# Kernel tuning notes

Hardware: AMD Instinct MI355X
Metric: run time of the kernel (lower is better)

## Reference

```python
import jax, jax.numpy as jnp
import numpy as np

B, N, D = 64, 577, 768
H = 12
HD = D // H
TOP_K_RATIO = 0.1


def setup_inputs() -> dict:
    key = jax.random.key(0)
    ks = jax.random.split(key, 8)
    s = 1.0 / np.sqrt(D)
    return {
        "x": jax.random.normal(ks[0], (B, N, D), jnp.float32),
        "accumulated_attention": jax.random.uniform(ks[1], (B, N, N), jnp.float32),
        "q_w": jax.random.normal(ks[2], (D, D), jnp.float32) * s,
        "k_w": jax.random.normal(ks[3], (D, D), jnp.float32) * s,
        "v_w": jax.random.normal(ks[4], (D, D), jnp.float32) * s,
        "proj_w": jax.random.normal(ks[5], (D, D), jnp.float32) * s,
        "proj_b": jnp.zeros((D,), jnp.float32),
    }


def reference(x, accumulated_attention, q_w, k_w, v_w, proj_w, proj_b):
    b, n, d = x.shape
    scale = HD ** -0.5
    # CLS-to-patch attention rollout row: (B, N-1)
    cls_attn = accumulated_attention[:, 0, 1:]
    # projections -> (B, H, N, HD)
    q = (x @ q_w.T).reshape(b, n, H, HD).transpose(0, 2, 1, 3)
    k = (x @ k_w.T).reshape(b, n, H, HD).transpose(0, 2, 1, 3)
    v = (x @ v_w.T).reshape(b, n, H, HD).transpose(0, 2, 1, 3)
    # top-k patch selection (+1 for CLS offset), prepend CLS index 0
    kk = max(1, int((n - 1) * TOP_K_RATIO))
    _, top_idx = jax.lax.top_k(cls_attn, kk)
    sel = jnp.concatenate([jnp.zeros((b, 1), top_idx.dtype), top_idx + 1], axis=1)  # (B, K+1)
    # gather selected queries: (B, H, K+1, HD)
    local_q = jnp.take_along_axis(q, sel[:, None, :, None], axis=2)
    # cross-attention of local queries against full K/V
    attn = jax.nn.softmax(jnp.einsum("bhkd,bhnd->bhkn", local_q, k) * scale, axis=-1)
    local_out = jnp.einsum("bhkn,bhnd->bhkd", attn, v)
    local_out = local_out.transpose(0, 2, 1, 3).reshape(b, -1, d)  # (B, K+1, D)
    # scatter back into a copy of x (indices are unique per batch)
    out = x.at[jnp.arange(b)[:, None], sel].set(local_out)
    return out @ proj_w.T + proj_b
```

## Files before the change

### kernel.cpp

```cpp
#include <hip/hip_runtime.h>
#include <stdint.h>

typedef unsigned short u16;
typedef short bf16x8 __attribute__((ext_vector_type(8)));
typedef float f32x4 __attribute__((ext_vector_type(4)));

__device__ __forceinline__ float b2f(u16 u){
  unsigned int i = ((unsigned int)u) << 16;
  return __builtin_bit_cast(float, i);
}
__device__ __forceinline__ u16 f2b(float f){
  unsigned int i = __builtin_bit_cast(unsigned int, f);
  i += 0x7FFFu + ((i >> 16) & 1u);
  return (u16)(i >> 16);
}

__device__ __forceinline__ void async16(const void* g, void* l){
  __builtin_amdgcn_global_load_lds((__attribute__((address_space(1))) void*)(void*)g,
                                   (__attribute__((address_space(3))) void*)l, 16, 0, 0);
}

__global__ void probe_kernel(const u16* __restrict__ qw, int* __restrict__ flag){
  int cnt = 0;
  for (int i = threadIdx.x; i < 4096; i += 64){
    int e = (qw[i] >> 7) & 0xFF;
    cnt += (e >= 140);
  }
#pragma unroll
  for (int off = 32; off; off >>= 1) cnt += __shfl_down(cnt, off);
  if (threadIdx.x == 0) *flag = (cnt > 64) ? 1 : 0;
}

__global__ __launch_bounds__(256) void cvt_kernel(const void* __restrict__ src,
                                                  u16* __restrict__ dst, int n,
                                                  const int* __restrict__ flagp){
  const int i = (blockIdx.x * 256 + threadIdx.x) * 8;
  if (i >= n) return;
  if (*flagp){
    f32x4 a = *(const f32x4*)((const float*)src + i);
    f32x4 b = *(const f32x4*)((const float*)src + i + 4);
    bf16x8 v;
#pragma unroll
    for (int j = 0; j < 4; ++j){ v[j] = (short)f2b(a[j]); v[4+j] = (short)f2b(b[j]); }
    *(bf16x8*)(dst + i) = v;
  } else {
    *(bf16x8*)(dst + i) = *(const bf16x8*)((const u16*)src + i);
  }
}

__global__ __launch_bounds__(256) void cvtw4_kernel(const void* __restrict__ s0,
                                                    const void* __restrict__ s1,
                                                    const void* __restrict__ s2,
                                                    const void* __restrict__ s3,
                                                    u16* __restrict__ dst,
                                                    const int* __restrict__ flagp){
  const int b = blockIdx.x;
  const int wsel = b / 288;
  const int i = (b - wsel*288) * 2048 + threadIdx.x * 8;
  const void* src = (wsel == 0) ? s0 : (wsel == 1) ? s1 : (wsel == 2) ? s2 : s3;
  u16* d = dst + (size_t)wsel * 589824 + i;
  if (*flagp){
    f32x4 a = *(const f32x4*)((const float*)src + i);
    f32x4 c = *(const f32x4*)((const float*)src + i + 4);
    bf16x8 v;
#pragma unroll
    for (int j = 0; j < 4; ++j){ v[j] = (short)f2b(a[j]); v[4+j] = (short)f2b(c[j]); }
    *(bf16x8*)d = v;
  } else {
    *(bf16x8*)d = *(const bf16x8*)((const u16*)src + i);
  }
}

__global__ void cvtb_kernel(const void* __restrict__ src, float* __restrict__ dst,
                            int n, const int* __restrict__ flagp){
  int i = blockIdx.x * 256 + threadIdx.x;
  if (i < n) dst[i] = *flagp ? ((const float*)src)[i] : b2f(((const u16*)src)[i]);
}

__global__ __launch_bounds__(576) void topk_kernel(const void* __restrict__ aa,
                                                   int* __restrict__ qrows,
                                                   const int* __restrict__ flagp){
  const int b = blockIdx.x;
  const int isf32 = *flagp;
  __shared__ float vals[576];
  const int i = threadIdx.x;
  const size_t off = (size_t)b*332929 + 1 + i;
  vals[i] = isf32 ? ((const float*)aa)[off] : b2f(((const u16*)aa)[off]);
  __syncthreads();
  const float vi = vals[i];
  int rank = 0;
  for (int j = 0; j < 576; ++j){
    float vj = vals[j];
    rank += (int)((vj > vi) || (vj == vi && j < i));
  }
  if (rank < 57) qrows[b*58 + 1 + rank] = b*577 + i + 1;
  if (i == 0)    qrows[b*58] = b*577;
}

__global__ __launch_bounds__(256) void gemm_bt(
    const u16* __restrict__ A, const u16* __restrict__ W,
    u16* __restrict__ Ck, u16* __restrict__ Cvt, float* __restrict__ Cout,
    u16* __restrict__ Clq,
    const int* __restrict__ qrows, const float* __restrict__ bias, int mode)
{
  __shared__ __align__(16) u16 As0[4096], As1[4096], As2[4096];
  __shared__ __align__(16) u16 Bs0[4096], Bs1[4096], Bs2[4096];
  const int tid = threadIdx.x;
  const int w = tid >> 6, l = tid & 63;

  int bx, by; bool lqp = false;
  if (mode == 0){
    const int bid = blockIdx.x;
    const int wg = (bid & 7) * 672 + (bid >> 3);
    if (wg < 5202){ bx = wg % 18; by = wg / 18; }
    else { const int t = wg - 5202; bx = t % 6; by = t / 6; lqp = true; }
  } else { bx = blockIdx.x; by = blockIdx.y; }

  const int mBase = by * 128;
  const int nBase = bx * 128;
  const int Meff  = (mode == 0 && !lqp) ? 36928 : 3712;

  const int r0 = tid >> 2;
  const int kc = (((tid & 3) ^ ((r0 >> 1) & 3)) * 8);
  int arow0 = mBase + r0;       if (arow0 > Meff-1) arow0 = Meff-1;
  int arow1 = mBase + 64 + r0;  if (arow1 > Meff-1) arow1 = Meff-1;
  if (mode == 0 && lqp){ arow0 = qrows[arow0]; arow1 = qrows[arow1]; }
  const int wrowBase = (mode == 0 && !lqp) ? (768 + nBase) : nBase;
  const u16* ag0 = A + (size_t)arow0 * 768 + kc;
  const u16* ag1 = A + (size_t)arow1 * 768 + kc;
  const u16* bg0 = W + (size_t)(wrowBase + r0) * 768 + kc;
  const u16* bg1 = W + (size_t)(wrowBase + 64 + r0) * 768 + kc;
  const int toff0 = tid * 8, toff1 = (256 + tid) * 8;

  f32x4 acc[4][4] = {};
  const int wm = (w >> 1) * 64, wn = (w & 1) * 64;
  const int lm = l & 15;
  const int lkx = (((l >> 4) ^ ((l >> 1) & 3)) * 8);

#define STAGE(Ab, Bb, koff) do { \
    async16(ag0 + (koff), &Ab[toff0]); \
    async16(ag1 + (koff), &Ab[toff1]); \
    async16(bg0 + (koff), &Bb[toff0]); \
    async16(bg1 + (koff), &Bb[toff1]); } while(0)

#define COMPUTE(Ab, Bb) { \
    bf16x8 af[4], bfr[4]; \
    _Pragma("unroll") \
    for (int i = 0; i < 4; ++i) af[i]  = *(const bf16x8*)&Ab[(wm + i*16 + lm)*32 + lkx]; \
    _Pragma("unroll") \
    for (int j = 0; j < 4; ++j) bfr[j] = *(const bf16x8*)&Bb[(wn + j*16 + lm)*32 + lkx]; \
    __builtin_amdgcn_s_setprio(1); \
    _Pragma("unroll") \
    for (int i = 0; i < 4; ++i) \
      _Pragma("unroll") \
      for (int j = 0; j < 4; ++j) \
        acc[i][j] = __builtin_amdgcn_mfma_f32_16x16x32_bf16(af[i], bfr[j], acc[i][j], 0, 0, 0); \
    __builtin_amdgcn_s_setprio(0); }

#define VMW4 asm volatile("s_waitcnt vmcnt(4)" ::: "memory")
#define VMW0 asm volatile("s_waitcnt vmcnt(0)" ::: "memory")
#define BAR  __builtin_amdgcn_s_barrier()

  STAGE(As0, Bs0, 0);
  STAGE(As1, Bs1, 32);
#pragma unroll
  for (int u = 0; u < 7; ++u){
    const int kb = u * 96;
    VMW4; BAR; STAGE(As2, Bs2, kb + 64);  COMPUTE(As0, Bs0);
    VMW4; BAR; STAGE(As0, Bs0, kb + 96);  COMPUTE(As1, Bs1);
    VMW4; BAR; STAGE(As1, Bs1, kb + 128); COMPUTE(As2, Bs2);
  }
  VMW4; BAR; STAGE(As2, Bs2, 736); COMPUTE(As0, Bs0);
  VMW4; BAR;                       COMPUTE(As1, Bs1);
  VMW0; BAR;                       COMPUTE(As2, Bs2);

#undef STAGE
#undef COMPUTE
#undef VMW4
#undef VMW0
#undef BAR

  if (mode == 1){
#pragma unroll
    for (int i = 0; i < 4; ++i){
#pragma unroll
      for (int r = 0; r < 4; ++r){
        int m = mBase + wm + i*16 + ((l >> 4) << 2) + r;
        if (m < 3712){
          size_t base = (size_t)qrows[m] * 768;
#pragma unroll
          for (int j = 0; j < 4; ++j){
            int n = nBase + wn + j*16 + lm;
            Cout[base + n] = acc[i][j][r] + bias[n];
          }
        }
      }
    }
    return;
  }
  if (lqp){
#pragma unroll
    for (int i = 0; i < 4; ++i){
#pragma unroll
      for (int r = 0; r < 4; ++r){
        int m = mBase + wm + i*16 + ((l >> 4) << 2) + r;
#pragma unroll
        for (int j = 0; j < 4; ++j){
          int n = nBase + wn + j*16 + lm;
          Clq[(size_t)m*768 + n] = f2b(acc[i][j][r]);
        }
      }
    }
  } else if (nBase < 768){
#pragma unroll
    for (int i = 0; i < 4; ++i){
#pragma unroll
      for (int r = 0; r < 4; ++r){
        int m = mBase + wm + i*16 + ((l >> 4) << 2) + r;
        if (m < 36928){
#pragma unroll
          for (int j = 0; j < 4; ++j){
            int n = nBase + wn + j*16 + lm;
            Ck[(size_t)m*768 + n] = f2b(acc[i][j][r]);
          }
        }
      }
    }
  } else if (nBase < 1536){
#pragma unroll
    for (int i = 0; i < 4; ++i){
#pragma unroll
      for (int r = 0; r < 4; ++r){
        int m = mBase + wm + i*16 + ((l >> 4) << 2) + r;
        if (m < 36928){
          int bb = m / 577;
          int nn = m - bb*577;
#pragma unroll
          for (int j = 0; j < 4; ++j){
            int nf = nBase - 768 + wn + j*16 + lm;
            Cvt[((size_t)(bb*12 + (nf >> 6))*64 + (nf & 63))*608 + nn] = f2b(acc[i][j][r]);
          }
        }
      }
    }
  } else {
#pragma unroll
    for (int i = 0; i < 4; ++i){
#pragma unroll
      for (int r = 0; r < 4; ++r){
        int m = mBase + wm + i*16 + ((l >> 4) << 2) + r;
        if (m < 36928){
          size_t base = (size_t)m * 768;
#pragma unroll
          for (int j = 0; j < 4; ++j){
            int nf = nBase - 1536 + wn + j*16 + lm;
            Cout[base + nf] = acc[i][j][r] + bias[nf];
          }
        }
      }
    }
  }
}

#define SLD 580
__global__ __launch_bounds__(256) void attn_kernel(
    const u16* __restrict__ lq, const u16* __restrict__ K,
    const u16* __restrict__ Vt, u16* __restrict__ lout)
{
  const int bid = blockIdx.x;
  const int wg = (bid & 7) * 384 + (bid >> 3);
  const int mt = wg & 3;
  const int hb = wg >> 2;
  const int h = hb % 12, b = hb / 12;

  __shared__ __align__(16) u16 qs[16*64];
  __shared__ __align__(16) float S[16*SLD];
  float* red = (float*)qs;
  const int tid = threadIdx.x, w = tid >> 6, l = tid & 63;
  const int lm = l & 15, lk = (l >> 4) * 8;

  for (int idx = tid; idx < 1024; idx += 256){
    int r = idx >> 6, c = idx & 63;
    int gm = mt*16 + r;
    qs[idx] = (gm < 58) ? lq[((size_t)b*58 + gm)*768 + h*64 + c] : (u16)0;
  }
  __syncthreads();
  bf16x8 aq0 = *(const bf16x8*)&qs[lm*64 + lk];
  bf16x8 aq1 = *(const bf16x8*)&qs[lm*64 + 32 + lk];

  const u16* Kb = K + (size_t)b*577*768 + h*64;
  for (int t = w; t < 37; t += 4){
    int n0 = t*16;
    int n = n0 + lm; if (n > 576) n = 576;
    const u16* kp = Kb + (size_t)n*768;
    bf16x8 b0 = *(const bf16x8*)&kp[lk];
    bf16x8 b1 = *(const bf16x8*)&kp[32 + lk];
    f32x4 c = {};
    c = __builtin_amdgcn_mfma_f32_16x16x32_bf16(aq0, b0, c, 0, 0, 0);
    c = __builtin_amdgcn_mfma_f32_16x16x32_bf16(aq1, b1, c, 0, 0, 0);
    if (n0 + lm < 577){
#pragma unroll
      for (int r = 0; r < 4; ++r)
        S[(((l >> 4) << 2) + r)*SLD + n0 + lm] = c[r] * 0.125f;
    }
  }
  __syncthreads();

  const int row = tid >> 4, g = tid & 15;
  float mx = -1e30f;
  for (int n = g; n < 577; n += 16) mx = fmaxf(mx, S[row*SLD + n]);
  red[row*17 + g] = mx;
  __syncthreads();
  float m2 = red[row*17];
#pragma unroll
  for (int i = 1; i < 16; ++i) m2 = fmaxf(m2, red[row*17 + i]);
  float sum = 0.f;
  for (int n = g; n < 577; n += 16){
    float e = __expf(S[row*SLD + n] - m2);
    S[row*SLD + n] = e;
    sum += e;
  }
  __syncthreads();
  red[row*17 + g] = sum;
  __syncthreads();
  float s2 = 0.f;
#pragma unroll
  for (int i = 0; i < 16; ++i) s2 += red[row*17 + i];
  float inv = 1.f / s2;
  for (int n = g; n < 577; n += 16) S[row*SLD + n] *= inv;
  __syncthreads();

  const u16* Vb = Vt + ((size_t)(b*12 + h) * 64) * 608;
  f32x4 oc = {};
  for (int ks = 0; ks < 18; ++ks){
    int kb = ks*32 + lk;
    f32x4 p0 = *(const f32x4*)&S[lm*SLD + kb];
    f32x4 p1 = *(const f32x4*)&S[lm*SLD + kb + 4];
    bf16x8 af;
#pragma unroll
    for (int j = 0; j < 4; ++j){ af[j] = (short)f2b(p0[j]); af[4+j] = (short)f2b(p1[j]); }
    bf16x8 bv = *(const bf16x8*)&Vb[(size_t)(w*16 + lm)*608 + kb];
    oc = __builtin_amdgcn_mfma_f32_16x16x32_bf16(af, bv, oc, 0, 0, 0);
  }
  {
    float vt576 = b2f(Vb[(size_t)(w*16 + lm)*608 + 576]);
#pragma unroll
    for (int r = 0; r < 4; ++r)
      oc[r] += S[(((l >> 4) << 2) + r)*SLD + 576] * vt576;
  }
#pragma unroll
  for (int r = 0; r < 4; ++r){
    int ml = mt*16 + ((l >> 4) << 2) + r;
    if (ml < 58)
      lout[((size_t)b*58 + ml)*768 + h*64 + w*16 + lm] = f2b(oc[r]);
  }
}

extern "C" void kernel_launch(void* const* d_in, const int* in_sizes, int n_in,
                              void* d_out, int out_size, void* d_ws, size_t ws_size,
                              hipStream_t stream)
{
  const void* x    = d_in[0];
  const void* aacc = d_in[1];
  const void* q_w  = d_in[2];
  const void* k_w  = d_in[3];
  const void* v_w  = d_in[4];
  const void* p_w  = d_in[5];
  const void* p_b  = d_in[6];

  const int M  = 36928;
  const int Ms = 3712;
  const int XE = M * 768;
  const int WE = 768 * 768;

  u16* Kbuf = (u16*)d_ws;
  u16* Vt   = Kbuf + (size_t)M * 768;
  u16* lq   = Vt + (size_t)768 * 64 * 608;
  u16* lout = lq + (size_t)Ms * 768;
  u16* xb   = lout + (size_t)Ms * 768;
  u16* qwb  = xb + (size_t)XE;
  u16* pwb  = qwb + (size_t)3 * WE;
  float* biasf = (float*)(qwb + (size_t)4 * WE);
  int* qrows = (int*)(biasf + 768);
  int* flagp = qrows + 3712;

  probe_kernel<<<1, 64, 0, stream>>>((const u16*)q_w, flagp);
  cvt_kernel<<<XE/8/256, 256, 0, stream>>>(x, xb, XE, flagp);
  cvtw4_kernel<<<1152, 256, 0, stream>>>(q_w, k_w, v_w, p_w, qwb, flagp);
  cvtb_kernel<<<3, 256, 0, stream>>>(p_b, biasf, 768, flagp);
  topk_kernel<<<64, 576, 0, stream>>>(aacc, qrows, flagp);

  gemm_bt<<<5376, 256, 0, stream>>>(xb, qwb, Kbuf, Vt, (float*)d_out, lq,
                                    qrows, biasf, 0);
  attn_kernel<<<3072, 256, 0, stream>>>(lq, Kbuf, Vt, lout);
  gemm_bt<<<dim3(6, 29), 256, 0, stream>>>(lout, pwb, nullptr, nullptr,
                                           (float*)d_out, nullptr, qrows, biasf, 1);
}
```

Measured before the change: 578.2 us.

## Fuse conversion kernels, widen attention blocks, and retune GEMM scheduling

Merges the probe, x, weight and bias conversion kernels into one prep kernel, with each block re-deriving the fp32/bf16 flag locally. The attention kernel moves to 512 threads: the K-dimension of P·V is split across two wave groups and reduced through shared memory, and softmax normalisation is deferred to the output. The GEMM gets a launch_bounds occupancy hint of 3 and a simpler block-to-tile mapping that separates the local-query tiles. This trades extra redundant flag reads and extra attention syncs for fewer launches and more parallelism.

```diff
diff --git a/kernel.cpp b/kernel.cpp
--- a/kernel.cpp
+++ b/kernel.cpp
@@ -20,68 +20,66 @@
                                    (__attribute__((address_space(3))) void*)l, 16, 0, 0);
 }
 
-__global__ void probe_kernel(const u16* __restrict__ qw, int* __restrict__ flag){
-  int cnt = 0;
-  for (int i = threadIdx.x; i < 4096; i += 64){
-    int e = (qw[i] >> 7) & 0xFF;
-    cnt += (e >= 140);
-  }
-#pragma unroll
-  for (int off = 32; off; off >>= 1) cnt += __shfl_down(cnt, off);
-  if (threadIdx.x == 0) *flag = (cnt > 64) ? 1 : 0;
-}
-
-__global__ __launch_bounds__(256) void cvt_kernel(const void* __restrict__ src,
-                                                  u16* __restrict__ dst, int n,
-                                                  const int* __restrict__ flagp){
-  const int i = (blockIdx.x * 256 + threadIdx.x) * 8;
-  if (i >= n) return;
-  if (*flagp){
-    f32x4 a = *(const f32x4*)((const float*)src + i);
-    f32x4 b = *(const f32x4*)((const float*)src + i + 4);
-    bf16x8 v;
-#pragma unroll
-    for (int j = 0; j < 4; ++j){ v[j] = (short)f2b(a[j]); v[4+j] = (short)f2b(b[j]); }
-    *(bf16x8*)(dst + i) = v;
+__device__ __forceinline__ int local_isf32(const u16* __restrict__ qw){
+  int c = 0;
+#pragma unroll
+  for (int j = 0; j < 32; ++j){
+    bf16x8 v = *(const bf16x8*)(qw + j*8);
+#pragma unroll
+    for (int k = 0; k < 8; ++k) c += ((((u16)v[k] >> 7) & 0xFF) >= 140);
+  }
+  return c > 20;
+}
+
+__global__ __launch_bounds__(256) void prep_kernel(
+    const void* __restrict__ x,
+    const void* __restrict__ s0, const void* __restrict__ s1,
+    const void* __restrict__ s2, const void* __restrict__ s3,
+    u16* __restrict__ xb, u16* __restrict__ wb, float* __restrict__ biasf,
+    const void* __restrict__ pb)
+{
+  const int bid = blockIdx.x, tid = threadIdx.x;
+  const int isf32 = local_isf32((const u16*)s0);
+
+  if (bid < 13848){
+    const int i = bid * 2048 + tid * 8;
+    if (isf32){
+      f32x4 a = *(const f32x4*)((const float*)x + i);
+      f32x4 b = *(const f32x4*)((const float*)x + i + 4);
+      bf16x8 v;
+#pragma unroll
+      for (int j = 0; j < 4; ++j){ v[j] = (short)f2b(a[j]); v[4+j] = (short)f2b(b[j]); }
+      *(bf16x8*)(xb + i) = v;
+    } else {
+      *(bf16x8*)(xb + i) = *(const bf16x8*)((const u16*)x + i);
+    }
+  } else if (bid < 15000){
+    const int b = bid - 13848;
+    const int wsel = b / 288;
+    const int i = (b - wsel*288) * 2048 + tid * 8;
+    const void* src = (wsel == 0) ? s0 : (wsel == 1) ? s1 : (wsel == 2) ? s2 : s3;
+    u16* d = wb + (size_t)wsel * 589824 + i;
+    if (isf32){
+      f32x4 a = *(const f32x4*)((const float*)src + i);
+      f32x4 c = *(const f32x4*)((const float*)src + i + 4);
+      bf16x8 v;
+#pragma unroll
+      for (int j = 0; j < 4; ++j){ v[j] = (short)f2b(a[j]); v[4+j] = (short)f2b(c[j]); }
+      *(bf16x8*)d = v;
+    } else {
+      *(bf16x8*)d = *(const bf16x8*)((const u16*)src + i);
+    }
   } else {
-    *(bf16x8*)(dst + i) = *(const bf16x8*)((const u16*)src + i);
-  }
-}
-
-__global__ __launch_bounds__(256) void cvtw4_kernel(const void* __restrict__ s0,
-                                                    const void* __restrict__ s1,
-                                                    const void* __restrict__ s2,
-                                                    const void* __restrict__ s3,
-                                                    u16* __restrict__ dst,
-                                                    const int* __restrict__ flagp){
-  const int b = blockIdx.x;
-  const int wsel = b / 288;
-  const int i = (b - wsel*288) * 2048 + threadIdx.x * 8;
-  const void* src = (wsel == 0) ? s0 : (wsel == 1) ? s1 : (wsel == 2) ? s2 : s3;
-  u16* d = dst + (size_t)wsel * 589824 + i;
-  if (*flagp){
-    f32x4 a = *(const f32x4*)((const float*)src + i);
-    f32x4 c = *(const f32x4*)((const float*)src + i + 4);
-    bf16x8 v;
-#pragma unroll
-    for (int j = 0; j < 4; ++j){ v[j] = (short)f2b(a[j]); v[4+j] = (short)f2b(c[j]); }
-    *(bf16x8*)d = v;
-  } else {
-    *(bf16x8*)d = *(const bf16x8*)((const u16*)src + i);
-  }
-}
-
-__global__ void cvtb_kernel(const void* __restrict__ src, float* __restrict__ dst,
-                            int n, const int* __restrict__ flagp){
-  int i = blockIdx.x * 256 + threadIdx.x;
-  if (i < n) dst[i] = *flagp ? ((const float*)src)[i] : b2f(((const u16*)src)[i]);
+    const int i = (bid - 15000) * 256 + tid;
+    if (i < 768) biasf[i] = isf32 ? ((const float*)pb)[i] : b2f(((const u16*)pb)[i]);
+  }
 }
 
 __global__ __launch_bounds__(576) void topk_kernel(const void* __restrict__ aa,
                                                    int* __restrict__ qrows,
-                                                   const int* __restrict__ flagp){
+                                                   const u16* __restrict__ qw){
   const int b = blockIdx.x;
-  const int isf32 = *flagp;
+  const int isf32 = local_isf32(qw);
   __shared__ float vals[576];
   const int i = threadIdx.x;
   const size_t off = (size_t)b*332929 + 1 + i;
@@ -97,7 +95,7 @@
   if (i == 0)    qrows[b*58] = b*577;
 }
 
-__global__ __launch_bounds__(256) void gemm_bt(
+__global__ __launch_bounds__(256, 3) void gemm_bt(
     const u16* __restrict__ A, const u16* __restrict__ W,
     u16* __restrict__ Ck, u16* __restrict__ Cvt, float* __restrict__ Cout,
     u16* __restrict__ Clq,
@@ -111,9 +109,11 @@
   int bx, by; bool lqp = false;
   if (mode == 0){
     const int bid = blockIdx.x;
-    const int wg = (bid & 7) * 672 + (bid >> 3);
-    if (wg < 5202){ bx = wg % 18; by = wg / 18; }
-    else { const int t = wg - 5202; bx = t % 6; by = t / 6; lqp = true; }
+    if (bid < 5202){
+      const int x = bid & 7, o = bid >> 3;
+      const int wg = (x < 2 ? x*651 : 2*651 + (x-2)*650) + o;
+      bx = wg % 18; by = wg / 18;
+    } else { const int t = bid - 5202; bx = t % 6; by = t / 6; lqp = true; }
   } else { bx = blockIdx.x; by = blockIdx.y; }
 
   const int mBase = by * 128;
@@ -165,10 +165,9 @@
   STAGE(As1, Bs1, 32);
 #pragma unroll
   for (int u = 0; u < 7; ++u){
-    const int kb = u * 96;
-    VMW4; BAR; STAGE(As2, Bs2, kb + 64);  COMPUTE(As0, Bs0);
-    VMW4; BAR; STAGE(As0, Bs0, kb + 96);  COMPUTE(As1, Bs1);
-    VMW4; BAR; STAGE(As1, Bs1, kb + 128); COMPUTE(As2, Bs2);
+    VMW4; BAR; STAGE(As2, Bs2, u*96 + 64);  COMPUTE(As0, Bs0);
+    VMW4; BAR; STAGE(As0, Bs0, u*96 + 96);  COMPUTE(As1, Bs1);
+    VMW4; BAR; STAGE(As1, Bs1, u*96 + 128); COMPUTE(As2, Bs2);
   }
   VMW4; BAR; STAGE(As2, Bs2, 736); COMPUTE(As0, Bs0);
   VMW4; BAR;                       COMPUTE(As1, Bs1);
@@ -263,7 +262,7 @@
 }
 
 #define SLD 580
-__global__ __launch_bounds__(256) void attn_kernel(
+__global__ __launch_bounds__(512) void attn_kernel(
     const u16* __restrict__ lq, const u16* __restrict__ K,
     const u16* __restrict__ Vt, u16* __restrict__ lout)
 {
@@ -275,11 +274,12 @@
 
   __shared__ __align__(16) u16 qs[16*64];
   __shared__ __align__(16) float S[16*SLD];
-  float* red = (float*)qs;
+  float* red  = (float*)qs;
+  float* invp = red + 16*17;
   const int tid = threadIdx.x, w = tid >> 6, l = tid & 63;
   const int lm = l & 15, lk = (l >> 4) * 8;
 
-  for (int idx = tid; idx < 1024; idx += 256){
+  for (int idx = tid; idx < 1024; idx += 512){
     int r = idx >> 6, c = idx & 63;
     int gm = mt*16 + r;
     qs[idx] = (gm < 58) ? lq[((size_t)b*58 + gm)*768 + h*64 + c] : (u16)0;
@@ -289,15 +289,15 @@
   bf16x8 aq1 = *(const bf16x8*)&qs[lm*64 + 32 + lk];
 
   const u16* Kb = K + (size_t)b*577*768 + h*64;
-  for (int t = w; t < 37; t += 4){
-    int n0 = t*16;
-    int n = n0 + lm; if (n > 576) n = 576;
+  for (int t = w; t < 37; t += 8){
+    int n = t*16 + lm; if (n > 576) n = 576;
     const u16* kp = Kb + (size_t)n*768;
     bf16x8 b0 = *(const bf16x8*)&kp[lk];
     bf16x8 b1 = *(const bf16x8*)&kp[32 + lk];
     f32x4 c = {};
     c = __builtin_amdgcn_mfma_f32_16x16x32_bf16(aq0, b0, c, 0, 0, 0);
     c = __builtin_amdgcn_mfma_f32_16x16x32_bf16(aq1, b1, c, 0, 0, 0);
+    const int n0 = t*16;
     if (n0 + lm < 577){
 #pragma unroll
       for (int r = 0; r < 4; ++r)
@@ -307,52 +307,70 @@
   __syncthreads();
 
   const int row = tid >> 4, g = tid & 15;
-  float mx = -1e30f;
-  for (int n = g; n < 577; n += 16) mx = fmaxf(mx, S[row*SLD + n]);
-  red[row*17 + g] = mx;
-  __syncthreads();
-  float m2 = red[row*17];
-#pragma unroll
-  for (int i = 1; i < 16; ++i) m2 = fmaxf(m2, red[row*17 + i]);
   float sum = 0.f;
-  for (int n = g; n < 577; n += 16){
-    float e = __expf(S[row*SLD + n] - m2);
-    S[row*SLD + n] = e;
-    sum += e;
-  }
-  __syncthreads();
-  red[row*17 + g] = sum;
-  __syncthreads();
-  float s2 = 0.f;
-#pragma unroll
-  for (int i = 0; i < 16; ++i) s2 += red[row*17 + i];
-  float inv = 1.f / s2;
-  for (int n = g; n < 577; n += 16) S[row*SLD + n] *= inv;
-  __syncthreads();
-
-  const u16* Vb = Vt + ((size_t)(b*12 + h) * 64) * 608;
+  if (tid < 256){
+    float mx = -1e30f;
+    for (int n = g; n < 577; n += 16) mx = fmaxf(mx, S[row*SLD + n]);
+    red[row*17 + g] = mx;
+  }
+  __syncthreads();
+  if (tid < 256){
+    float m2 = red[row*17];
+#pragma unroll
+    for (int i = 1; i < 16; ++i) m2 = fmaxf(m2, red[row*17 + i]);
+    for (int n = g; n < 577; n += 16){
+      float e = __expf(S[row*SLD + n] - m2);
+      S[row*SLD + n] = e;
+      sum += e;
+    }
+  }
+  __syncthreads();
+  if (tid < 256) red[row*17 + g] = sum;
+  __syncthreads();
+  if (tid < 256 && g == 0){
+    float s2 = 0.f;
+#pragma unroll
+    for (int i = 0; i < 16; ++i) s2 += red[row*17 + i];
+    invp[row] = 1.f / s2;
+  }
+  __syncthreads();
+
+  const u16* Vrow = Vt + (((size_t)(b*12 + h) * 64) + (w & 3)*16 + lm) * 608;
+  const int ksbeg = (w >> 2) * 9;
   f32x4 oc = {};
-  for (int ks = 0; ks < 18; ++ks){
-    int kb = ks*32 + lk;
+  for (int i = 0; i < 9; ++i){
+    const int kb = (ksbeg + i)*32 + lk;
     f32x4 p0 = *(const f32x4*)&S[lm*SLD + kb];
     f32x4 p1 = *(const f32x4*)&S[lm*SLD + kb + 4];
     bf16x8 af;
 #pragma unroll
     for (int j = 0; j < 4; ++j){ af[j] = (short)f2b(p0[j]); af[4+j] = (short)f2b(p1[j]); }
-    bf16x8 bv = *(const bf16x8*)&Vb[(size_t)(w*16 + lm)*608 + kb];
+    bf16x8 bv = *(const bf16x8*)&Vrow[kb];
     oc = __builtin_amdgcn_mfma_f32_16x16x32_bf16(af, bv, oc, 0, 0, 0);
   }
-  {
-    float vt576 = b2f(Vb[(size_t)(w*16 + lm)*608 + 576]);
+  if (w < 4){
+    float vt576 = b2f(Vrow[576]);
 #pragma unroll
     for (int r = 0; r < 4; ++r)
       oc[r] += S[(((l >> 4) << 2) + r)*SLD + 576] * vt576;
   }
-#pragma unroll
-  for (int r = 0; r < 4; ++r){
-    int ml = mt*16 + ((l >> 4) << 2) + r;
-    if (ml < 58)
-      lout[((size_t)b*58 + ml)*768 + h*64 + w*16 + lm] = f2b(oc[r]);
+  __syncthreads();
+  if (w >= 4){
+    float* scr = (float*)S;
+#pragma unroll
+    for (int r = 0; r < 4; ++r) scr[(w - 4)*256 + l*4 + r] = oc[r];
+  }
+  __syncthreads();
+  if (w < 4){
+    const float* scr = (const float*)S;
+#pragma unroll
+    for (int r = 0; r < 4; ++r){
+      int sr = (((l >> 4) << 2) + r);
+      float v = (oc[r] + scr[w*256 + l*4 + r]) * invp[sr];
+      int ml = mt*16 + sr;
+      if (ml < 58)
+        lout[((size_t)b*58 + ml)*768 + h*64 + (w & 3)*16 + lm] = f2b(v);
+    }
   }
 }
 
@@ -382,17 +400,13 @@
   u16* pwb  = qwb + (size_t)3 * WE;
   float* biasf = (float*)(qwb + (size_t)4 * WE);
   int* qrows = (int*)(biasf + 768);
-  int* flagp = qrows + 3712;
-
-  probe_kernel<<<1, 64, 0, stream>>>((const u16*)q_w, flagp);
-  cvt_kernel<<<XE/8/256, 256, 0, stream>>>(x, xb, XE, flagp);
-  cvtw4_kernel<<<1152, 256, 0, stream>>>(q_w, k_w, v_w, p_w, qwb, flagp);
-  cvtb_kernel<<<3, 256, 0, stream>>>(p_b, biasf, 768, flagp);
-  topk_kernel<<<64, 576, 0, stream>>>(aacc, qrows, flagp);
+
+  prep_kernel<<<15003, 256, 0, stream>>>(x, q_w, k_w, v_w, p_w, xb, qwb, biasf, p_b);
+  topk_kernel<<<64, 576, 0, stream>>>(aacc, qrows, (const u16*)q_w);
 
   gemm_bt<<<5376, 256, 0, stream>>>(xb, qwb, Kbuf, Vt, (float*)d_out, lq,
                                     qrows, biasf, 0);
-  attn_kernel<<<3072, 256, 0, stream>>>(lq, Kbuf, Vt, lout);
+  attn_kernel<<<3072, 512, 0, stream>>>(lq, Kbuf, Vt, lout);
   gemm_bt<<<dim3(6, 29), 256, 0, stream>>>(lout, pwb, nullptr, nullptr,
                                            (float*)d_out, nullptr, qrows, biasf, 1);
 }
```

Measured after the change: 600.4 us. +3.8%, slower.
